# Kernel optimization log

Hardware: AMD Instinct MI355X
Metric: run time of the kernel (lower is better)

## Reference

```python
import jax, jax.numpy as jnp
import numpy as np

B, H, S, DK = 2, 8, 4096, 64


def setup_inputs() -> dict:
    key = jax.random.key(0)
    kq, kk, kv = jax.random.split(key, 3)
    Q = jax.random.normal(kq, (B, H, S, DK), dtype=jnp.float32)
    K = jax.random.normal(kk, (B, H, S, DK), dtype=jnp.float32)
    V = jax.random.normal(kv, (B, H, S, DK), dtype=jnp.float32)
    attn_mask = jnp.zeros((1,), dtype=bool)  # accepted but unused by the module
    return {"Q": Q, "K": K, "V": V, "attn_mask": attn_mask}


def reference(Q, K, V, attn_mask):
    d_k = Q.shape[-1]
    scale = 1.0 / np.sqrt(d_k).astype(np.float32)
    # scores: [b, h, q, k] -- full O(n^2) matrix, as in the original
    scores = jnp.einsum('bhqd,bhkd->bhqk', Q, K) * scale
    attn = jax.nn.softmax(scores, axis=-1)
    context = jnp.einsum('bhqk,bhkd->bhqd', attn, V)
    return (context, attn)
```

## Files before the change

kernel.cpp:

```cpp
#include <hip/hip_runtime.h>
#include <hip/hip_bf16.h>


typedef __bf16 bf16x8 __attribute__((ext_vector_type(8)));
typedef __bf16 bf16x4 __attribute__((ext_vector_type(4)));
typedef float f32x4 __attribute__((ext_vector_type(4)));

#define BH 16
#define SEQ 4096
#define DKD 64
#define PSTRIDE 72

__global__ void cvt_bf16_kernel(const float* __restrict__ src,
                                __bf16* __restrict__ dst, int n4, float scale) {
    int i = blockIdx.x * blockDim.x + threadIdx.x;
    if (i < n4) {
        const float4 v = reinterpret_cast<const float4*>(src)[i];
        bf16x4 o;
        o[0] = (__bf16)(v.x * scale); o[1] = (__bf16)(v.y * scale);
        o[2] = (__bf16)(v.z * scale); o[3] = (__bf16)(v.w * scale);
        reinterpret_cast<bf16x4*>(dst)[i] = o;
    }
}

__global__ void transpose_v_kernel(const float* __restrict__ V,
                                   __bf16* __restrict__ Vt) {
    __shared__ __bf16 T[DKD][72];
    const int head = blockIdx.y;
    const int s0 = blockIdx.x * 64;
    const int t = threadIdx.x;
    const float* vp = V + ((size_t)head * SEQ + s0) * DKD;
#pragma unroll
    for (int i = 0; i < 16; ++i) {
        int j = i * 256 + t;
        T[j & 63][j >> 6] = (__bf16)vp[j];
    }
    __syncthreads();
    __bf16* op = Vt + (size_t)head * DKD * SEQ + s0;
#pragma unroll
    for (int i = 0; i < 16; ++i) {
        int j = i * 256 + t;
        op[(size_t)(j >> 6) * SEQ + (j & 63)] = T[j >> 6][j & 63];
    }
}

__global__ __launch_bounds__(128) void attn_kernel(
    const __bf16* __restrict__ Qb, const __bf16* __restrict__ Kb,
    const __bf16* __restrict__ Vt, float* __restrict__ out_ctx,
    float* __restrict__ out_attn) {
    __shared__ __align__(16) __bf16 Pl[2][2][16][PSTRIDE];

    const int tid = threadIdx.x;
    const int w = tid >> 6;
    const int lane = tid & 63;
    const int c16 = lane & 15;
    const int g = lane >> 4;
    const int head = blockIdx.y;
    const int qbase = blockIdx.x * 32 + w * 16;

    const __bf16* qp = Qb + ((size_t)head * SEQ + qbase + c16) * DKD + g * 8;
    const bf16x8 qf0 = *reinterpret_cast<const bf16x8*>(qp);
    const bf16x8 qf1 = *reinterpret_cast<const bf16x8*>(qp + 32);

    const __bf16* kbase = Kb + (size_t)head * SEQ * DKD;
    const __bf16* vbase = Vt + (size_t)head * DKD * SEQ;
    float* attn_p = out_attn + ((size_t)head * SEQ + qbase) * SEQ;

    float lsum = 0.f;
    for (int kt = 0; kt < SEQ; kt += 64) {
        f32x4 acc[4];
#pragma unroll
        for (int ct = 0; ct < 4; ++ct) {
            acc[ct] = (f32x4){0.f, 0.f, 0.f, 0.f};
            const __bf16* kp = kbase + (size_t)(kt + ct * 16 + c16) * DKD + g * 8;
            bf16x8 kf0 = *reinterpret_cast<const bf16x8*>(kp);
            bf16x8 kf1 = *reinterpret_cast<const bf16x8*>(kp + 32);
            acc[ct] = __builtin_amdgcn_mfma_f32_16x16x32_bf16(kf0, qf0, acc[ct], 0, 0, 0);
            acc[ct] = __builtin_amdgcn_mfma_f32_16x16x32_bf16(kf1, qf1, acc[ct], 0, 0, 0);
        }
#pragma unroll
        for (int ct = 0; ct < 4; ++ct) {
            float e0 = __builtin_amdgcn_exp2f(acc[ct][0]);
            float e1 = __builtin_amdgcn_exp2f(acc[ct][1]);
            float e2 = __builtin_amdgcn_exp2f(acc[ct][2]);
            float e3 = __builtin_amdgcn_exp2f(acc[ct][3]);
            lsum += (e0 + e1) + (e2 + e3);
        }
    }
    lsum += __shfl_xor(lsum, 16);
    lsum += __shfl_xor(lsum, 32);
    float inv_l = __builtin_amdgcn_rcpf(lsum);

    f32x4 o[4];
#pragma unroll
    for (int dt = 0; dt < 4; ++dt) o[dt] = (f32x4){0.f, 0.f, 0.f, 0.f};

    auto computeS = [&](int tile, __bf16(*Pbuf)[PSTRIDE]) {
        const int kt = tile * 64;
        f32x4 acc[4];
#pragma unroll
        for (int ct = 0; ct < 4; ++ct) {
            acc[ct] = (f32x4){0.f, 0.f, 0.f, 0.f};
            const __bf16* kp = kbase + (size_t)(kt + ct * 16 + c16) * DKD + g * 8;
            bf16x8 kf0 = *reinterpret_cast<const bf16x8*>(kp);
            bf16x8 kf1 = *reinterpret_cast<const bf16x8*>(kp + 32);
            acc[ct] = __builtin_amdgcn_mfma_f32_16x16x32_bf16(kf0, qf0, acc[ct], 0, 0, 0);
            acc[ct] = __builtin_amdgcn_mfma_f32_16x16x32_bf16(kf1, qf1, acc[ct], 0, 0, 0);
        }
#pragma unroll
        for (int ct = 0; ct < 4; ++ct) {
            f32x4 p;
#pragma unroll
            for (int r = 0; r < 4; ++r)
                p[r] = __builtin_amdgcn_exp2f(acc[ct][r]) * inv_l;
            __builtin_nontemporal_store(
                p, reinterpret_cast<f32x4*>(attn_p + (size_t)c16 * SEQ + kt + ct * 16 + g * 4));
            bf16x4 pb;
#pragma unroll
            for (int r = 0; r < 4; ++r) pb[r] = (__bf16)p[r];
            *reinterpret_cast<bf16x4*>(&Pbuf[c16][ct * 16 + g * 4]) = pb;
        }
    };

    auto pvTile = [&](int tile, const __bf16(*Pbuf)[PSTRIDE]) {
        const int kt = tile * 64;
        bf16x8 pb0 = *reinterpret_cast<const bf16x8*>(&Pbuf[c16][g * 8]);
        bf16x8 pb1 = *reinterpret_cast<const bf16x8*>(&Pbuf[c16][g * 8 + 32]);
#pragma unroll
        for (int dt = 0; dt < 4; ++dt) {
            const __bf16* vp = vbase + (size_t)(dt * 16 + c16) * SEQ + kt + g * 8;
            bf16x8 vf0 = *reinterpret_cast<const bf16x8*>(vp);
            bf16x8 vf1 = *reinterpret_cast<const bf16x8*>(vp + 32);
            o[dt] = __builtin_amdgcn_mfma_f32_16x16x32_bf16(vf0, pb0, o[dt], 0, 0, 0);
            o[dt] = __builtin_amdgcn_mfma_f32_16x16x32_bf16(vf1, pb1, o[dt], 0, 0, 0);
        }
    };

    computeS(0, Pl[0][w]);
    for (int t = 1; t < 63; t += 2) {
        computeS(t, Pl[1][w]);
        pvTile(t - 1, Pl[0][w]);
        computeS(t + 1, Pl[0][w]);
        pvTile(t, Pl[1][w]);
    }
    computeS(63, Pl[1][w]);
    pvTile(62, Pl[0][w]);
    pvTile(63, Pl[1][w]);

    float* ctx_p = out_ctx + ((size_t)head * SEQ + qbase) * DKD;
#pragma unroll
    for (int dt = 0; dt < 4; ++dt)
        *reinterpret_cast<f32x4*>(ctx_p + (size_t)c16 * DKD + dt * 16 + g * 4) = o[dt];
}

extern "C" void kernel_launch(void* const* d_in, const int* in_sizes, int n_in,
                              void* d_out, int out_size, void* d_ws, size_t ws_size,
                              hipStream_t stream) {
    const float* Q = (const float*)d_in[0];
    const float* K = (const float*)d_in[1];
    const float* V = (const float*)d_in[2];
    float* out = (float*)d_out;

    const size_t nElem = (size_t)BH * SEQ * DKD;
    __bf16* Qb = (__bf16*)d_ws;
    __bf16* Kb = Qb + nElem;
    __bf16* Vt = Kb + nElem;

    float* out_ctx = out;
    float* out_attn = out + nElem;

    const int n4 = (int)(nElem / 4);
    cvt_bf16_kernel<<<dim3((n4 + 255) / 256), dim3(256), 0, stream>>>(
        Q, Qb, n4, 0.125f * 1.44269504088896f);
    cvt_bf16_kernel<<<dim3((n4 + 255) / 256), dim3(256), 0, stream>>>(K, Kb, n4, 1.0f);
    transpose_v_kernel<<<dim3(64, BH), dim3(256), 0, stream>>>(V, Vt);
    attn_kernel<<<dim3(SEQ / 32, BH), dim3(128), 0, stream>>>(Qb, Kb, Vt, out_ctx, out_attn);
}
```

Baseline: 734.8 us.

## Coalesce attention-matrix stores through LDS, widen blocks, swizzle heads, prefetch K

Each score tile is now restaged through the per-wave LDS buffer, so each group of 16 lanes writes a 256-byte contiguous row segment of the attention matrix instead of scattered 64-byte pieces. The row-sum pass double-buffers K fragments in registers to hide load latency. Blocks grow to 4 waves with a flat grid that interleaves heads across blocks, and the log2e factor moves from the Q pre-scale into the exp argument. In exchange, the stored attention probabilities are now bf16-rounded values widened back to fp32, which lowers output precision, and each exp costs an extra multiply.

```diff
diff --git a/kernel.cpp b/kernel.cpp
--- a/kernel.cpp
+++ b/kernel.cpp
@@ -10,6 +10,7 @@
 #define SEQ 4096
 #define DKD 64
 #define PSTRIDE 72
+#define LOG2E 1.44269504088896f
 
 __global__ void cvt_bf16_kernel(const float* __restrict__ src,
                                 __bf16* __restrict__ dst, int n4, float scale) {
@@ -44,19 +45,22 @@
     }
 }
 
-__global__ __launch_bounds__(128) void attn_kernel(
+__global__ __launch_bounds__(256, 4) void attn_kernel(
     const __bf16* __restrict__ Qb, const __bf16* __restrict__ Kb,
     const __bf16* __restrict__ Vt, float* __restrict__ out_ctx,
     float* __restrict__ out_attn) {
-    __shared__ __align__(16) __bf16 Pl[2][2][16][PSTRIDE];
+    __shared__ __align__(16) __bf16 Pl[2][4][16][PSTRIDE];
 
     const int tid = threadIdx.x;
     const int w = tid >> 6;
     const int lane = tid & 63;
     const int c16 = lane & 15;
     const int g = lane >> 4;
-    const int head = blockIdx.y;
-    const int qbase = blockIdx.x * 32 + w * 16;
+
+    const int wg = blockIdx.x;
+    const int head = ((wg & 7) << 1) | ((wg >> 3) & 1);
+    const int qt = wg >> 4;
+    const int qbase = qt * 64 + w * 16;
 
     const __bf16* qp = Qb + ((size_t)head * SEQ + qbase + c16) * DKD + g * 8;
     const bf16x8 qf0 = *reinterpret_cast<const bf16x8*>(qp);
@@ -67,7 +71,48 @@
     float* attn_p = out_attn + ((size_t)head * SEQ + qbase) * SEQ;
 
     float lsum = 0.f;
-    for (int kt = 0; kt < SEQ; kt += 64) {
+    auto loadK = [&](bf16x8 (&kf)[8], int tile) {
+        const int kt = tile * 64;
+#pragma unroll
+        for (int ct = 0; ct < 4; ++ct) {
+            const __bf16* kp = kbase + (size_t)(kt + ct * 16 + c16) * DKD + g * 8;
+            kf[ct * 2] = *reinterpret_cast<const bf16x8*>(kp);
+            kf[ct * 2 + 1] = *reinterpret_cast<const bf16x8*>(kp + 32);
+        }
+    };
+    auto procA = [&](const bf16x8 (&kf)[8]) {
+#pragma unroll
+        for (int ct = 0; ct < 4; ++ct) {
+            f32x4 a = (f32x4){0.f, 0.f, 0.f, 0.f};
+            a = __builtin_amdgcn_mfma_f32_16x16x32_bf16(kf[ct * 2], qf0, a, 0, 0, 0);
+            a = __builtin_amdgcn_mfma_f32_16x16x32_bf16(kf[ct * 2 + 1], qf1, a, 0, 0, 0);
+            float e0 = __builtin_amdgcn_exp2f(a[0] * LOG2E);
+            float e1 = __builtin_amdgcn_exp2f(a[1] * LOG2E);
+            float e2 = __builtin_amdgcn_exp2f(a[2] * LOG2E);
+            float e3 = __builtin_amdgcn_exp2f(a[3] * LOG2E);
+            lsum += (e0 + e1) + (e2 + e3);
+        }
+    };
+    {
+        bf16x8 kA[8], kB[8];
+        loadK(kA, 0);
+        for (int t = 0; t < 64; t += 2) {
+            loadK(kB, t + 1);
+            procA(kA);
+            loadK(kA, (t + 2) & 63);
+            procA(kB);
+        }
+    }
+    lsum += __shfl_xor(lsum, 16);
+    lsum += __shfl_xor(lsum, 32);
+    const float inv_l = __builtin_amdgcn_rcpf(lsum);
+
+    f32x4 o[4];
+#pragma unroll
+    for (int dt = 0; dt < 4; ++dt) o[dt] = (f32x4){0.f, 0.f, 0.f, 0.f};
+
+    auto computeS = [&](int tile, __bf16(*Pbuf)[PSTRIDE]) {
+        const int kt = tile * 64;
         f32x4 acc[4];
 #pragma unroll
         for (int ct = 0; ct < 4; ++ct) {
@@ -80,45 +125,25 @@
         }
 #pragma unroll
         for (int ct = 0; ct < 4; ++ct) {
-            float e0 = __builtin_amdgcn_exp2f(acc[ct][0]);
-            float e1 = __builtin_amdgcn_exp2f(acc[ct][1]);
-            float e2 = __builtin_amdgcn_exp2f(acc[ct][2]);
-            float e3 = __builtin_amdgcn_exp2f(acc[ct][3]);
-            lsum += (e0 + e1) + (e2 + e3);
-        }
-    }
-    lsum += __shfl_xor(lsum, 16);
-    lsum += __shfl_xor(lsum, 32);
-    float inv_l = __builtin_amdgcn_rcpf(lsum);
-
-    f32x4 o[4];
-#pragma unroll
-    for (int dt = 0; dt < 4; ++dt) o[dt] = (f32x4){0.f, 0.f, 0.f, 0.f};
-
-    auto computeS = [&](int tile, __bf16(*Pbuf)[PSTRIDE]) {
-        const int kt = tile * 64;
-        f32x4 acc[4];
-#pragma unroll
-        for (int ct = 0; ct < 4; ++ct) {
-            acc[ct] = (f32x4){0.f, 0.f, 0.f, 0.f};
-            const __bf16* kp = kbase + (size_t)(kt + ct * 16 + c16) * DKD + g * 8;
-            bf16x8 kf0 = *reinterpret_cast<const bf16x8*>(kp);
-            bf16x8 kf1 = *reinterpret_cast<const bf16x8*>(kp + 32);
-            acc[ct] = __builtin_amdgcn_mfma_f32_16x16x32_bf16(kf0, qf0, acc[ct], 0, 0, 0);
-            acc[ct] = __builtin_amdgcn_mfma_f32_16x16x32_bf16(kf1, qf1, acc[ct], 0, 0, 0);
-        }
-#pragma unroll
-        for (int ct = 0; ct < 4; ++ct) {
-            f32x4 p;
+            bf16x4 pb;
 #pragma unroll
             for (int r = 0; r < 4; ++r)
-                p[r] = __builtin_amdgcn_exp2f(acc[ct][r]) * inv_l;
+                pb[r] = (__bf16)(__builtin_amdgcn_exp2f(acc[ct][r] * LOG2E) * inv_l);
+            *reinterpret_cast<bf16x4*>(&Pbuf[c16][ct * 16 + g * 4]) = pb;
+        }
+    };
+
+    auto storeAttn = [&](int tile, const __bf16(*Pbuf)[PSTRIDE]) {
+        const int kt = tile * 64;
+#pragma unroll
+        for (int r4 = 0; r4 < 4; ++r4) {
+            const int row = r4 * 4 + g;
+            bf16x4 pb = *reinterpret_cast<const bf16x4*>(&Pbuf[row][c16 * 4]);
+            f32x4 v;
+#pragma unroll
+            for (int j = 0; j < 4; ++j) v[j] = (float)pb[j];
             __builtin_nontemporal_store(
-                p, reinterpret_cast<f32x4*>(attn_p + (size_t)c16 * SEQ + kt + ct * 16 + g * 4));
-            bf16x4 pb;
-#pragma unroll
-            for (int r = 0; r < 4; ++r) pb[r] = (__bf16)p[r];
-            *reinterpret_cast<bf16x4*>(&Pbuf[c16][ct * 16 + g * 4]) = pb;
+                v, reinterpret_cast<f32x4*>(attn_p + (size_t)row * SEQ + kt + c16 * 4));
         }
     };
 
@@ -139,12 +164,16 @@
     computeS(0, Pl[0][w]);
     for (int t = 1; t < 63; t += 2) {
         computeS(t, Pl[1][w]);
+        storeAttn(t - 1, Pl[0][w]);
         pvTile(t - 1, Pl[0][w]);
         computeS(t + 1, Pl[0][w]);
+        storeAttn(t, Pl[1][w]);
         pvTile(t, Pl[1][w]);
     }
     computeS(63, Pl[1][w]);
+    storeAttn(62, Pl[0][w]);
     pvTile(62, Pl[0][w]);
+    storeAttn(63, Pl[1][w]);
     pvTile(63, Pl[1][w]);
 
     float* ctx_p = out_ctx + ((size_t)head * SEQ + qbase) * DKD;
@@ -170,9 +199,8 @@
     float* out_attn = out + nElem;
 
     const int n4 = (int)(nElem / 4);
-    cvt_bf16_kernel<<<dim3((n4 + 255) / 256), dim3(256), 0, stream>>>(
-        Q, Qb, n4, 0.125f * 1.44269504088896f);
+    cvt_bf16_kernel<<<dim3((n4 + 255) / 256), dim3(256), 0, stream>>>(Q, Qb, n4, 0.125f);
     cvt_bf16_kernel<<<dim3((n4 + 255) / 256), dim3(256), 0, stream>>>(K, Kb, n4, 1.0f);
     transpose_v_kernel<<<dim3(64, BH), dim3(256), 0, stream>>>(V, Vt);
-    attn_kernel<<<dim3(SEQ / 32, BH), dim3(128), 0, stream>>>(Qb, Kb, Vt, out_ctx, out_attn);
-}
+    attn_kernel<<<dim3(BH * SEQ / 64), dim3(256), 0, stream>>>(Qb, Kb, Vt, out_ctx, out_attn);
+}
```

New measurement: 728.6 us. Within noise of the previous version (-0.8%).

## Remap grid to 1D with head swizzle, add occupancy hint, split score tiles

Applied to the files above, without the earlier changes.

Flattens the launch grid to 1D and swizzles blocks so consecutive workgroups cover different heads, which spreads K/V traffic across L2/XCD partitions. Adds a min-blocks-per-CU hint to launch_bounds and processes each 64-key score tile as two 32-key halves to lower register pressure. It also replaces the nontemporal attn stores with regular stores. The log2e factor moves from the Q prescale into a per-element multiply, which adds a multiply per exp and changes bf16 rounding of Q slightly.

```diff
diff --git a/kernel.cpp b/kernel.cpp
--- a/kernel.cpp
+++ b/kernel.cpp
@@ -10,6 +10,7 @@
 #define SEQ 4096
 #define DKD 64
 #define PSTRIDE 72
+#define LOG2E 1.44269504088896f
 
 __global__ void cvt_bf16_kernel(const float* __restrict__ src,
                                 __bf16* __restrict__ dst, int n4, float scale) {
@@ -44,7 +45,7 @@
     }
 }
 
-__global__ __launch_bounds__(128) void attn_kernel(
+__global__ __launch_bounds__(128, 5) void attn_kernel(
     const __bf16* __restrict__ Qb, const __bf16* __restrict__ Kb,
     const __bf16* __restrict__ Vt, float* __restrict__ out_ctx,
     float* __restrict__ out_attn) {
@@ -55,8 +56,11 @@
     const int lane = tid & 63;
     const int c16 = lane & 15;
     const int g = lane >> 4;
-    const int head = blockIdx.y;
-    const int qbase = blockIdx.x * 32 + w * 16;
+
+    const int wg = blockIdx.x;
+    const int head = ((wg & 7) << 1) | ((wg >> 3) & 1);
+    const int qblk = wg >> 4;
+    const int qbase = qblk * 32 + w * 16;
 
     const __bf16* qp = Qb + ((size_t)head * SEQ + qbase + c16) * DKD + g * 8;
     const bf16x8 qf0 = *reinterpret_cast<const bf16x8*>(qp);
@@ -67,63 +71,64 @@
     float* attn_p = out_attn + ((size_t)head * SEQ + qbase) * SEQ;
 
     float lsum = 0.f;
-    for (int kt = 0; kt < SEQ; kt += 64) {
-        f32x4 acc[4];
+    for (int t = 0; t < 64; ++t) {
+        const int kt = t * 64;
 #pragma unroll
         for (int ct = 0; ct < 4; ++ct) {
-            acc[ct] = (f32x4){0.f, 0.f, 0.f, 0.f};
             const __bf16* kp = kbase + (size_t)(kt + ct * 16 + c16) * DKD + g * 8;
             bf16x8 kf0 = *reinterpret_cast<const bf16x8*>(kp);
             bf16x8 kf1 = *reinterpret_cast<const bf16x8*>(kp + 32);
-            acc[ct] = __builtin_amdgcn_mfma_f32_16x16x32_bf16(kf0, qf0, acc[ct], 0, 0, 0);
-            acc[ct] = __builtin_amdgcn_mfma_f32_16x16x32_bf16(kf1, qf1, acc[ct], 0, 0, 0);
-        }
-#pragma unroll
-        for (int ct = 0; ct < 4; ++ct) {
-            float e0 = __builtin_amdgcn_exp2f(acc[ct][0]);
-            float e1 = __builtin_amdgcn_exp2f(acc[ct][1]);
-            float e2 = __builtin_amdgcn_exp2f(acc[ct][2]);
-            float e3 = __builtin_amdgcn_exp2f(acc[ct][3]);
+            f32x4 a = (f32x4){0.f, 0.f, 0.f, 0.f};
+            a = __builtin_amdgcn_mfma_f32_16x16x32_bf16(kf0, qf0, a, 0, 0, 0);
+            a = __builtin_amdgcn_mfma_f32_16x16x32_bf16(kf1, qf1, a, 0, 0, 0);
+            float e0 = __builtin_amdgcn_exp2f(a[0] * LOG2E);
+            float e1 = __builtin_amdgcn_exp2f(a[1] * LOG2E);
+            float e2 = __builtin_amdgcn_exp2f(a[2] * LOG2E);
+            float e3 = __builtin_amdgcn_exp2f(a[3] * LOG2E);
             lsum += (e0 + e1) + (e2 + e3);
         }
     }
     lsum += __shfl_xor(lsum, 16);
     lsum += __shfl_xor(lsum, 32);
-    float inv_l = __builtin_amdgcn_rcpf(lsum);
+    const float inv_l = __builtin_amdgcn_rcpf(lsum);
 
     f32x4 o[4];
 #pragma unroll
     for (int dt = 0; dt < 4; ++dt) o[dt] = (f32x4){0.f, 0.f, 0.f, 0.f};
 
-    auto computeS = [&](int tile, __bf16(*Pbuf)[PSTRIDE]) {
-        const int kt = tile * 64;
-        f32x4 acc[4];
+    auto computeS = [&](int t, __bf16(*Pbuf)[PSTRIDE]) {
+        const int kt = t * 64;
 #pragma unroll
-        for (int ct = 0; ct < 4; ++ct) {
-            acc[ct] = (f32x4){0.f, 0.f, 0.f, 0.f};
-            const __bf16* kp = kbase + (size_t)(kt + ct * 16 + c16) * DKD + g * 8;
-            bf16x8 kf0 = *reinterpret_cast<const bf16x8*>(kp);
-            bf16x8 kf1 = *reinterpret_cast<const bf16x8*>(kp + 32);
-            acc[ct] = __builtin_amdgcn_mfma_f32_16x16x32_bf16(kf0, qf0, acc[ct], 0, 0, 0);
-            acc[ct] = __builtin_amdgcn_mfma_f32_16x16x32_bf16(kf1, qf1, acc[ct], 0, 0, 0);
-        }
+        for (int h = 0; h < 2; ++h) {
+            f32x4 acc[2];
 #pragma unroll
-        for (int ct = 0; ct < 4; ++ct) {
-            f32x4 p;
+            for (int ct = 0; ct < 2; ++ct) {
+                acc[ct] = (f32x4){0.f, 0.f, 0.f, 0.f};
+                const __bf16* kp =
+                    kbase + (size_t)(kt + h * 32 + ct * 16 + c16) * DKD + g * 8;
+                bf16x8 kf0 = *reinterpret_cast<const bf16x8*>(kp);
+                bf16x8 kf1 = *reinterpret_cast<const bf16x8*>(kp + 32);
+                acc[ct] = __builtin_amdgcn_mfma_f32_16x16x32_bf16(kf0, qf0, acc[ct], 0, 0, 0);
+                acc[ct] = __builtin_amdgcn_mfma_f32_16x16x32_bf16(kf1, qf1, acc[ct], 0, 0, 0);
+            }
 #pragma unroll
-            for (int r = 0; r < 4; ++r)
-                p[r] = __builtin_amdgcn_exp2f(acc[ct][r]) * inv_l;
-            __builtin_nontemporal_store(
-                p, reinterpret_cast<f32x4*>(attn_p + (size_t)c16 * SEQ + kt + ct * 16 + g * 4));
-            bf16x4 pb;
+            for (int ct = 0; ct < 2; ++ct) {
+                f32x4 p;
+                bf16x4 pb;
 #pragma unroll
-            for (int r = 0; r < 4; ++r) pb[r] = (__bf16)p[r];
-            *reinterpret_cast<bf16x4*>(&Pbuf[c16][ct * 16 + g * 4]) = pb;
+                for (int r = 0; r < 4; ++r) {
+                    p[r] = __builtin_amdgcn_exp2f(acc[ct][r] * LOG2E) * inv_l;
+                    pb[r] = (__bf16)p[r];
+                }
+                *reinterpret_cast<f32x4*>(
+                    attn_p + (size_t)c16 * SEQ + kt + h * 32 + ct * 16 + g * 4) = p;
+                *reinterpret_cast<bf16x4*>(&Pbuf[c16][h * 32 + ct * 16 + g * 4]) = pb;
+            }
         }
     };
 
-    auto pvTile = [&](int tile, const __bf16(*Pbuf)[PSTRIDE]) {
-        const int kt = tile * 64;
+    auto pvTile = [&](int t, const __bf16(*Pbuf)[PSTRIDE]) {
+        const int kt = t * 64;
         bf16x8 pb0 = *reinterpret_cast<const bf16x8*>(&Pbuf[c16][g * 8]);
         bf16x8 pb1 = *reinterpret_cast<const bf16x8*>(&Pbuf[c16][g * 8 + 32]);
 #pragma unroll
@@ -170,9 +175,8 @@
     float* out_attn = out + nElem;
 
     const int n4 = (int)(nElem / 4);
-    cvt_bf16_kernel<<<dim3((n4 + 255) / 256), dim3(256), 0, stream>>>(
-        Q, Qb, n4, 0.125f * 1.44269504088896f);
+    cvt_bf16_kernel<<<dim3((n4 + 255) / 256), dim3(256), 0, stream>>>(Q, Qb, n4, 0.125f);
     cvt_bf16_kernel<<<dim3((n4 + 255) / 256), dim3(256), 0, stream>>>(K, Kb, n4, 1.0f);
     transpose_v_kernel<<<dim3(64, BH), dim3(256), 0, stream>>>(V, Vt);
-    attn_kernel<<<dim3(SEQ / 32, BH), dim3(128), 0, stream>>>(Qb, Kb, Vt, out_ctx, out_attn);
+    attn_kernel<<<dim3(BH * SEQ / 32), dim3(128), 0, stream>>>(Qb, Kb, Vt, out_ctx, out_attn);
 }
```

After: 803.7 us. 1.09x slower.
